# Optimization experiments

Hardware: AMD Instinct MI355X
Metric: run time of the kernel (lower is better)

## Reference

```python
import jax, jax.numpy as jnp
import numpy as np

N_OBJ = 8192
N_FLOOR = 8192
R = 0.001          # particles_radius
DT = 0.01
STEPS = 100
SLEEP_TH = DT * 9.8


def setup_inputs() -> dict:
    key = jax.random.key(0)
    k1, k2 = jax.random.split(key)
    # object point cloud hovering slightly above the floor plane (z in [0.02, 0.22])
    obj_pc = jax.random.uniform(k1, (N_OBJ, 3), dtype=jnp.float32) * 0.2
    obj_pc = obj_pc.at[:, 2].add(0.02)
    # fixed floor particles sampled on the z=0 plane
    xy = jax.random.uniform(k2, (N_FLOOR, 2), dtype=jnp.float32) * 0.4 - 0.1
    floor_pc = jnp.concatenate([xy, jnp.zeros((N_FLOOR, 1), jnp.float32)], axis=1)
    return {"obj_pc": obj_pc, "floor_pc": floor_pc, "iter_step": 0, "obj_idx": 0}


def _simulate(obj_pc, floor_pc):
    """Rigid-body (translation) drop under gravity with particle-particle floor contact.
    Tracks each particle's position at its first collision and a collision mask."""
    g = jnp.array([0.0, 0.0, -9.8], dtype=obj_pc.dtype)
    up = jnp.array([0.0, 0.0, 1.0], dtype=obj_pc.dtype)
    xy_keep = jnp.array([1.0, 1.0, 0.0], dtype=obj_pc.dtype)

    def step(carry, _):
        t, v, p_first, collided, asleep = carry
        # compute_rigid_motion_wo_contact: semi-implicit Euler on rigid translation
        v_n = v + g * DT
        t_n = t + v_n * DT
        p = obj_pc + t_n                                   # [N,3] world positions
        # proximity_detection_with_fix_particles: min dist to any floor particle
        d2 = jnp.sum((p[:, None, :] - floor_pc[None, :, :]) ** 2, axis=-1)  # [N,M]
        dmin = jnp.sqrt(jnp.min(d2, axis=1) + 1e-12)       # [N]
        pen = 2.0 * R - dmin                               # penetration depth
        in_contact = pen > 0.0
        any_c = jnp.any(in_contact)
        max_pen = jnp.max(jnp.where(in_contact, pen, 0.0))
        # post_contact: project body out of penetration, kill vertical velocity
        t_c = t_n + jnp.where(any_c, max_pen, 0.0) * up
        v_c = jnp.where(any_c, v_n * xy_keep, v_n)
        p_c = obj_pc + t_c
        newly = in_contact & (~collided)
        p_first_n = jnp.where(newly[:, None], p_c, p_first)
        collided_n = collided | in_contact
        # check_sleep: stop once in contact and slow enough
        asleep_n = asleep | (any_c & (jnp.linalg.norm(v_c) < SLEEP_TH))
        # freeze all state once asleep (early-break equivalent)
        sel = lambda old, new: jnp.where(asleep, old, new)
        carry = (sel(t, t_c), sel(v, v_c), sel(p_first, p_first_n),
                 jnp.where(asleep, collided, collided_n), asleep_n)
        return carry, None

    carry0 = (jnp.zeros(3, obj_pc.dtype), jnp.zeros(3, obj_pc.dtype),
              obj_pc, jnp.zeros(obj_pc.shape[0], dtype=bool), jnp.array(False))
    (t, v, p_first, collided, asleep), _ = jax.lax.scan(
        jax.checkpoint(step), carry0, None, length=STEPS)
    return p_first, collided


def reference(obj_pc, floor_pc, iter_step, obj_idx):
    output_p_x, collision_mask = _simulate(obj_pc, floor_pc)
    return output_p_x, collision_mask
```

## Files before the change

### kernel.cpp

```cpp
#include <hip/hip_runtime.h>
#include <math.h>

#define N_OBJ   8192
#define N_FLOOR 8192
#define STEPS   100
#define DT      0.01f
#define GDT     (-9.8f * 0.01f)
#define TWO_R   0.002f
#define EPS12   1e-12f
#define BIGF    3.4e38f


__global__ __launch_bounds__(256) void floor_min_xy_k(
    const float* __restrict__ obj, const float* __restrict__ flr,
    unsigned int* __restrict__ ws_u) {
    __shared__ float2 sf[128];
    const int t = threadIdx.x;
    const int jbase = blockIdx.y * 128;
    if (t < 128) {
        int j = jbase + t;
        sf[t] = make_float2(flr[3 * j], flr[3 * j + 1]);
    }
    __syncthreads();
    const int ib = blockIdx.x * 1024;
    float x[4], y[4], m[4];
    #pragma unroll
    for (int c = 0; c < 4; ++c) {
        int i = ib + t + c * 256;
        x[c] = obj[3 * i];
        y[c] = obj[3 * i + 1];
        m[c] = BIGF;
    }
    #pragma unroll 4
    for (int j = 0; j < 128; ++j) {
        const float fx = sf[j].x, fy = sf[j].y;
        #pragma unroll
        for (int c = 0; c < 4; ++c) {
            float dx = x[c] - fx;
            float dy = y[c] - fy;
            float d = __fadd_rn(__fmul_rn(dx, dx), __fmul_rn(dy, dy));
            m[c] = fminf(m[c], d);
        }
    }
    #pragma unroll
    for (int c = 0; c < 4; ++c)
        atomicMax(&ws_u[ib + t + c * 256], ~__float_as_uint(m[c]));
}

__global__ __launch_bounds__(64) void first_contact_k(
    const float* __restrict__ obj, unsigned int* __restrict__ ws_u) {
    const int i = blockIdx.x * 64 + threadIdx.x;
    const float z = obj[3 * i + 2];
    const float dxy2 = __uint_as_float(~ws_u[i]);
    float v = 0.f, t = 0.f;
    unsigned long long key = ~0ull;
    for (int k = 1; k <= STEPS; ++k) {
        v = __fadd_rn(v, GDT);
        t = __fadd_rn(t, __fmul_rn(v, DT));
        float dz = __fadd_rn(z, t);
        float d2 = __fadd_rn(dxy2, __fmul_rn(dz, dz));
        float dmin = sqrtf(__fadd_rn(d2, EPS12));
        if (dmin < TWO_R) {
            key = ((unsigned long long)k << 32) | (unsigned int)__float_as_uint(d2);
            break;
        }
    }
    #pragma unroll
    for (int off = 32; off; off >>= 1) {
        unsigned long long o = __shfl_down(key, off, 64);
        key = (o < key) ? o : key;
    }
    if (threadIdx.x == 0)
        atomicMax((unsigned long long*)&ws_u[N_OBJ], ~key);
}

__global__ __launch_bounds__(256) void write_out_k(
    const float* __restrict__ obj, const unsigned int* __restrict__ ws_u,
    float* __restrict__ out) {
    const int i = blockIdx.x * 256 + threadIdx.x;
    const unsigned long long key = ~(*(const unsigned long long*)&ws_u[N_OBJ]);
    const unsigned int kstar = (unsigned int)(key >> 32);
    const float x = obj[3 * i], y = obj[3 * i + 1], z = obj[3 * i + 2];
    float outz = z;
    float mask = 0.f;
    if (kstar <= STEPS) {
        float v = 0.f, t = 0.f;
        for (unsigned int k = 1; k <= kstar; ++k) {
            v = __fadd_rn(v, GDT);
            t = __fadd_rn(t, __fmul_rn(v, DT));
        }
        const float d2min = __uint_as_float((unsigned int)(key & 0xFFFFFFFFu));
        const float dminmin = sqrtf(__fadd_rn(d2min, EPS12));
        const float maxpen = __fsub_rn(TWO_R, dminmin);
        const float tc = __fadd_rn(t, maxpen);
        const float dxy2 = __uint_as_float(~ws_u[i]);
        const float dz = __fadd_rn(z, t);
        const float d2 = __fadd_rn(dxy2, __fmul_rn(dz, dz));
        const float dmin = sqrtf(__fadd_rn(d2, EPS12));
        if (dmin < TWO_R) {
            outz = __fadd_rn(z, tc);
            mask = 1.f;
        }
    }
    out[3 * i]     = x;
    out[3 * i + 1] = y;
    out[3 * i + 2] = outz;
    out[3 * N_OBJ + i] = mask;
}

extern "C" void kernel_launch(void* const* d_in, const int* in_sizes, int n_in,
                              void* d_out, int out_size, void* d_ws, size_t ws_size,
                              hipStream_t stream) {
    const float* obj = (const float*)d_in[0];
    const float* flr = (const float*)d_in[1];
    unsigned int* ws_u = (unsigned int*)d_ws;
    float* out = (float*)d_out;

    floor_min_xy_k<<<dim3(8, 64), dim3(256), 0, stream>>>(obj, flr, ws_u);
    first_contact_k<<<dim3(128), dim3(64), 0, stream>>>(obj, ws_u);
    write_out_k<<<dim3(32), dim3(256), 0, stream>>>(obj, ws_u, out);
}
```

Measured before the change: 81.67 us.

## Fuse first-contact and write-out kernels using a grid-wide atomic barrier

Merges the first-contact search and the output-writing kernels into one launch of 32 blocks. Blocks reduce their keys through shared memory, publish them with an atomic max, then spin on a global counter until all blocks have arrived before reading the global key. The first kernel resets the counter. This removes one kernel launch and its gap, at the cost of a spin barrier that assumes all 32 blocks are resident at once.

```diff
diff --git a/kernel.cpp b/kernel.cpp
--- a/kernel.cpp
+++ b/kernel.cpp
@@ -16,6 +16,8 @@
     unsigned int* __restrict__ ws_u) {
     __shared__ float2 sf[128];
     const int t = threadIdx.x;
+    if (blockIdx.x == 0 && blockIdx.y == 0 && t == 0)
+        atomicExch(&ws_u[N_OBJ + 2], 0u);
     const int jbase = blockIdx.y * 128;
     if (t < 128) {
         int j = jbase + t;
@@ -47,11 +49,14 @@
         atomicMax(&ws_u[ib + t + c * 256], ~__float_as_uint(m[c]));
 }
 
-__global__ __launch_bounds__(64) void first_contact_k(
-    const float* __restrict__ obj, unsigned int* __restrict__ ws_u) {
-    const int i = blockIdx.x * 64 + threadIdx.x;
-    const float z = obj[3 * i + 2];
+__global__ __launch_bounds__(256) void contact_out_k(
+    const float* __restrict__ obj, unsigned int* __restrict__ ws_u,
+    float* __restrict__ out) {
+    __shared__ unsigned long long wkey[4];
+    const int i = blockIdx.x * 256 + threadIdx.x;
+    const float x = obj[3 * i], y = obj[3 * i + 1], z = obj[3 * i + 2];
     const float dxy2 = __uint_as_float(~ws_u[i]);
+
     float v = 0.f, t = 0.f;
     unsigned long long key = ~0ull;
     for (int k = 1; k <= STEPS; ++k) {
@@ -61,7 +66,7 @@
         float d2 = __fadd_rn(dxy2, __fmul_rn(dz, dz));
         float dmin = sqrtf(__fadd_rn(d2, EPS12));
         if (dmin < TWO_R) {
-            key = ((unsigned long long)k << 32) | (unsigned int)__float_as_uint(d2);
+            key = ((unsigned long long)k << 32) | (unsigned long long)__float_as_uint(d2);
             break;
         }
     }
@@ -70,31 +75,38 @@
         unsigned long long o = __shfl_down(key, off, 64);
         key = (o < key) ? o : key;
     }
-    if (threadIdx.x == 0)
-        atomicMax((unsigned long long*)&ws_u[N_OBJ], ~key);
-}
+    const int wv = threadIdx.x >> 6;
+    if ((threadIdx.x & 63) == 0) wkey[wv] = key;
+    __syncthreads();
+    unsigned long long* key64 = (unsigned long long*)&ws_u[N_OBJ];
+    unsigned int* ctr = &ws_u[N_OBJ + 2];
+    if (threadIdx.x == 0) {
+        unsigned long long bk = wkey[0];
+        #pragma unroll
+        for (int w = 1; w < 4; ++w) bk = (wkey[w] < bk) ? wkey[w] : bk;
+        atomicMax(key64, ~bk);
+        __hip_atomic_fetch_add(ctr, 1u, __ATOMIC_ACQ_REL, __HIP_MEMORY_SCOPE_AGENT);
+        while (__hip_atomic_load(ctr, __ATOMIC_ACQUIRE, __HIP_MEMORY_SCOPE_AGENT) < 32u)
+            __builtin_amdgcn_s_sleep(8);
+    }
+    __syncthreads();
 
-__global__ __launch_bounds__(256) void write_out_k(
-    const float* __restrict__ obj, const unsigned int* __restrict__ ws_u,
-    float* __restrict__ out) {
-    const int i = blockIdx.x * 256 + threadIdx.x;
-    const unsigned long long key = ~(*(const unsigned long long*)&ws_u[N_OBJ]);
-    const unsigned int kstar = (unsigned int)(key >> 32);
-    const float x = obj[3 * i], y = obj[3 * i + 1], z = obj[3 * i + 2];
+    const unsigned long long gkey =
+        ~__hip_atomic_load(key64, __ATOMIC_RELAXED, __HIP_MEMORY_SCOPE_AGENT);
+    const unsigned int kstar = (unsigned int)(gkey >> 32);
     float outz = z;
     float mask = 0.f;
     if (kstar <= STEPS) {
-        float v = 0.f, t = 0.f;
+        float vv = 0.f, tt = 0.f;
         for (unsigned int k = 1; k <= kstar; ++k) {
-            v = __fadd_rn(v, GDT);
-            t = __fadd_rn(t, __fmul_rn(v, DT));
+            vv = __fadd_rn(vv, GDT);
+            tt = __fadd_rn(tt, __fmul_rn(vv, DT));
         }
-        const float d2min = __uint_as_float((unsigned int)(key & 0xFFFFFFFFu));
+        const float d2min = __uint_as_float((unsigned int)(gkey & 0xFFFFFFFFu));
         const float dminmin = sqrtf(__fadd_rn(d2min, EPS12));
         const float maxpen = __fsub_rn(TWO_R, dminmin);
-        const float tc = __fadd_rn(t, maxpen);
-        const float dxy2 = __uint_as_float(~ws_u[i]);
-        const float dz = __fadd_rn(z, t);
+        const float tc = __fadd_rn(tt, maxpen);
+        const float dz = __fadd_rn(z, tt);
         const float d2 = __fadd_rn(dxy2, __fmul_rn(dz, dz));
         const float dmin = sqrtf(__fadd_rn(d2, EPS12));
         if (dmin < TWO_R) {
@@ -117,6 +129,5 @@
     float* out = (float*)d_out;
 
     floor_min_xy_k<<<dim3(8, 64), dim3(256), 0, stream>>>(obj, flr, ws_u);
-    first_contact_k<<<dim3(128), dim3(64), 0, stream>>>(obj, ws_u);
-    write_out_k<<<dim3(32), dim3(256), 0, stream>>>(obj, ws_u, out);
+    contact_out_k<<<dim3(32), dim3(256), 0, stream>>>(obj, ws_u, out);
 }
```

Result: no change. 82.86 us (+1.5%).
